# Optimization experiments

Hardware: AMD Instinct MI355X
Metric: run time of the kernel (lower is better)

The kernel has to match this reference:

```python
import jax, jax.numpy as jnp
import numpy as np

D_MODEL = 768
N_HEADS = 8
D_K = D_MODEL // N_HEADS
D_FF = 2048
EPS = 1e-5


def _layer_norm(x, gamma, beta):
    mu = jnp.mean(x, axis=-1, keepdims=True)
    var = jnp.mean(jnp.square(x - mu), axis=-1, keepdims=True)
    return (x - mu) * jax.lax.rsqrt(var + EPS) * gamma + beta


def setup_inputs() -> dict:
    key = jax.random.key(0)
    ks = jax.random.split(key, 16)
    s = 1.0 / np.sqrt(D_MODEL)
    sf = 1.0 / np.sqrt(D_FF)
    inp = {
        "x": jax.random.normal(ks[0], (4, 2048, D_MODEL), jnp.float32),
        "Wq": jax.random.uniform(ks[1], (D_MODEL, D_MODEL), jnp.float32, -s, s),
        "bq": jnp.zeros((D_MODEL,), jnp.float32),
        "Wk": jax.random.uniform(ks[2], (D_MODEL, D_MODEL), jnp.float32, -s, s),
        "bk": jnp.zeros((D_MODEL,), jnp.float32),
        "Wv": jax.random.uniform(ks[3], (D_MODEL, D_MODEL), jnp.float32, -s, s),
        "bv": jnp.zeros((D_MODEL,), jnp.float32),
        "Wo": jax.random.uniform(ks[4], (D_MODEL, D_MODEL), jnp.float32, -s, s),
        "bo": jnp.zeros((D_MODEL,), jnp.float32),
        "g1": jnp.ones((D_MODEL,), jnp.float32),
        "be1": jnp.zeros((D_MODEL,), jnp.float32),
        "W1": jax.random.uniform(ks[5], (D_MODEL, D_FF), jnp.float32, -s, s),
        "b1": jnp.zeros((D_FF,), jnp.float32),
        "W2": jax.random.uniform(ks[6], (D_FF, D_MODEL), jnp.float32, -sf, sf),
        "b2": jnp.zeros((D_MODEL,), jnp.float32),
        "g2": jnp.ones((D_MODEL,), jnp.float32),
        "be2": jnp.zeros((D_MODEL,), jnp.float32),
    }
    return inp


def reference(x, Wq, bq, Wk, bk, Wv, bv, Wo, bo, g1, be1, W1, b1, W2, b2, g2, be2):
    B, S, D = x.shape
    residual = x
    # projections, split into heads: [B, H, S, d_k]
    def proj(W, b):
        return (x @ W + b).reshape(B, S, N_HEADS, D_K).transpose(0, 2, 1, 3)
    Q, K, V = proj(Wq, bq), proj(Wk, bk), proj(Wv, bv)
    # explicit (non-fused) attention, as in the original
    scores = jnp.einsum('bhqd,bhkd->bhqk', Q, K) / np.sqrt(D_K)  # [B,H,S,S]
    attn = jax.nn.softmax(scores, axis=-1)
    out = jnp.einsum('bhqk,bhkd->bhqd', attn, V)
    out = out.transpose(0, 2, 1, 3).reshape(B, S, D)
    out = out @ Wo + bo
    x1 = _layer_norm(residual + out, g1, be1)
    ff = jax.nn.relu(x1 @ W1 + b1) @ W2 + b2
    return _layer_norm(x1 + ff, g2, be2)
```

## Files before the change

kernel.cpp:

```cpp
#include <hip/hip_runtime.h>
#include <cstdint>
#include <cstddef>

typedef unsigned short u16;
typedef __bf16 bf16x8 __attribute__((ext_vector_type(8)));
typedef float f32x4 __attribute__((ext_vector_type(4)));

#define BATCH 4
#define SEQ   2048
#define DM    768
#define NH    8
#define DK    96
#define DFF   2048
#define MTOK  8192
#define QKVN  2304
#define LOG2E 1.44269504088896340736f

__device__ __forceinline__ u16 f2bf(float f) {
  union { float f; uint32_t u; } v; v.f = f;
  return (u16)((v.u + 0x7fffu + ((v.u >> 16) & 1u)) >> 16);
}
__device__ __forceinline__ float bf2f(u16 b) {
  union { uint32_t u; float f; } v; v.u = (uint32_t)b << 16;
  return v.f;
}
__device__ __forceinline__ bf16x8 ld8(const u16* p) { return *(const bf16x8*)p; }
__device__ __forceinline__ void async16(const u16* g, u16* l) {
  __builtin_amdgcn_global_load_lds((const __attribute__((address_space(1))) void*)g,
                                   (__attribute__((address_space(3))) void*)l, 16, 0, 0);
}

__global__ __launch_bounds__(256)
void prep(const float* __restrict__ x, u16* __restrict__ xb,
          const float* __restrict__ bq, const float* __restrict__ bk,
          const float* __restrict__ bv, float* __restrict__ bqkv,
          const float* __restrict__ Wq, const float* __restrict__ Wk,
          const float* __restrict__ Wv, const float* __restrict__ Wo,
          const float* __restrict__ W1, const float* __restrict__ W2,
          u16* __restrict__ WT, u16* __restrict__ WoT,
          u16* __restrict__ W1T, u16* __restrict__ W2T) {
  __shared__ float t[32][33];
  const int tid = threadIdx.x;
  int bid = blockIdx.x;

  if (bid < 6144) {
    size_t i = (size_t)bid * 1024 + tid * 4;
    float4 f = *(const float4*)(x + i);
    uint2 o;
    o.x = (unsigned)f2bf(f.x) | ((unsigned)f2bf(f.y) << 16);
    o.y = (unsigned)f2bf(f.z) | ((unsigned)f2bf(f.w) << 16);
    *(uint2*)(xb + i) = o;
    return;
  }
  if (bid < 6153) {
    int i = (bid - 6144) * 256 + tid;
    float v = (i < 768) ? bq[i] : (i < 1536) ? bk[i - 768] : bv[i - 1536];
    bqkv[i] = v;
    return;
  }
  bid -= 6153;
  const float* in; u16* out; int C, R, bx, by;
  if (bid < 576)       { in = Wq; out = WT;                 C = 768;  R = 768;  bx = bid % 24;          by = bid / 24; }
  else if (bid < 1152) { in = Wk; out = WT + 768 * 768;     C = 768;  R = 768;  bx = (bid - 576) % 24;  by = (bid - 576) / 24; }
  else if (bid < 1728) { in = Wv; out = WT + 2 * 768 * 768; C = 768;  R = 768;  bx = (bid - 1152) % 24; by = (bid - 1152) / 24; }
  else if (bid < 2304) { in = Wo; out = WoT;                C = 768;  R = 768;  bx = (bid - 1728) % 24; by = (bid - 1728) / 24; }
  else if (bid < 3840) { in = W1; out = W1T;                C = 2048; R = 768;  bx = (bid - 2304) % 64; by = (bid - 2304) / 64; }
  else                 { in = W2; out = W2T;                C = 768;  R = 2048; bx = (bid - 3840) % 24; by = (bid - 3840) / 24; }
  const int r0 = by * 32, c0 = bx * 32;
  const int tx = tid & 31, ty = tid >> 5;
#pragma unroll
  for (int i = 0; i < 4; i++)
    t[ty + i * 8][tx] = in[(size_t)(r0 + ty + i * 8) * C + c0 + tx];
  __syncthreads();
#pragma unroll
  for (int i = 0; i < 4; i++)
    out[(size_t)(c0 + ty + i * 8) * R + r0 + tx] = f2bf(t[tx][ty + i * 8]);
}

__global__ void transpose_v(const u16* __restrict__ v, u16* __restrict__ vt) {
  __shared__ u16 t[32][33];
  int bh = blockIdx.z, b = bh >> 3, h = bh & 7;
  int s0 = blockIdx.x * 32, d0 = blockIdx.y * 32;
  int tx = threadIdx.x, ty = threadIdx.y;
#pragma unroll
  for (int i = 0; i < 4; i++)
    t[ty + i * 8][tx] = v[(size_t)(b * SEQ + s0 + ty + i * 8) * QKVN + h * DK + d0 + tx];
  __syncthreads();
#pragma unroll
  for (int i = 0; i < 4; i++)
    vt[(size_t)(bh * DK + d0 + ty + i * 8) * SEQ + s0 + tx] = t[tx][ty + i * 8];
}

template <int RESID, int RELU, int OUTBF>
__global__ __launch_bounds__(256, 4)
void gemm_bt(const u16* __restrict__ A, const u16* __restrict__ BT,
             const float* __restrict__ bias, const float* __restrict__ resid,
             float* __restrict__ Cf, u16* __restrict__ Cb, int N, int K) {
  __shared__ __align__(16) u16 lA[128 * 64];
  __shared__ __align__(16) u16 lB[128 * 64];
  const int tid = threadIdx.x;
  const int wave = tid >> 6, lane = tid & 63;
  const int quad = lane >> 4, l16 = lane & 15;
  const int wm = wave >> 1, wn = wave & 1;
  const int tm = blockIdx.y * 128, tn = blockIdx.x * 128;

  f32x4 acc[4][4] = {};

  for (int k0 = 0; k0 < K; k0 += 64) {
    __syncthreads();
#pragma unroll
    for (int i = 0; i < 4; i++) {
      int cbase = (wave * 4 + i) * 64;
      int c = cbase + lane;
      int row = c >> 3;
      int scc = (c & 7) ^ (row & 7);
      async16(A + (size_t)(tm + row) * K + k0 + scc * 8, &lA[cbase * 8]);
      async16(BT + (size_t)(tn + row) * K + k0 + scc * 8, &lB[cbase * 8]);
    }
    __syncthreads();
#pragma unroll
    for (int ks = 0; ks < 2; ks++) {
      bf16x8 af[4], bfr[4];
#pragma unroll
      for (int i = 0; i < 4; i++) {
        int ra = wm * 64 + i * 16 + l16;
        af[i] = ld8(&lA[ra * 64 + (((ks * 4 + quad) ^ (ra & 7)) << 3)]);
        int rb = wn * 64 + i * 16 + l16;
        bfr[i] = ld8(&lB[rb * 64 + (((ks * 4 + quad) ^ (rb & 7)) << 3)]);
      }
#pragma unroll
      for (int i = 0; i < 4; i++)
#pragma unroll
        for (int j = 0; j < 4; j++)
          acc[i][j] = __builtin_amdgcn_mfma_f32_16x16x32_bf16(af[i], bfr[j], acc[i][j], 0, 0, 0);
    }
  }

#pragma unroll
  for (int i = 0; i < 4; i++) {
    const int row0 = tm + wm * 64 + i * 16 + quad * 4;
#pragma unroll
    for (int j = 0; j < 4; j++) {
      const int col = tn + wn * 64 + j * 16 + l16;
      const float bv = bias[col];
#pragma unroll
      for (int r = 0; r < 4; r++) {
        float v = acc[i][j][r] + bv;
        if (RESID) v += resid[(size_t)(row0 + r) * N + col];
        if (RELU) v = fmaxf(v, 0.f);
        if (OUTBF) Cb[(size_t)(row0 + r) * N + col] = f2bf(v);
        else       Cf[(size_t)(row0 + r) * N + col] = v;
      }
    }
  }
}

template <int RESID, int RELU, int OUTBF, int RESBF>
__global__ __launch_bounds__(256, 4)
void gemm_bt64(const u16* __restrict__ A, const u16* __restrict__ BT,
               const float* __restrict__ bias, const float* __restrict__ residf,
               const u16* __restrict__ residb,
               float* __restrict__ Cf, u16* __restrict__ Cb, int N, int K) {
  __shared__ __align__(16) u16 lA[128 * 64];
  __shared__ __align__(16) u16 lB[64 * 64];
  const int tid = threadIdx.x;
  const int wave = tid >> 6, lane = tid & 63;
  const int quad = lane >> 4, l16 = lane & 15;
  const int wm = wave >> 1, wn = wave & 1;
  const int tm = blockIdx.y * 128, tn = blockIdx.x * 64;

  f32x4 acc[4][2] = {};

  for (int k0 = 0; k0 < K; k0 += 64) {
    __syncthreads();
#pragma unroll
    for (int i = 0; i < 4; i++) {
      int cbase = (wave * 4 + i) * 64;
      int c = cbase + lane;
      int row = c >> 3;
      int scc = (c & 7) ^ (row & 7);
      async16(A + (size_t)(tm + row) * K + k0 + scc * 8, &lA[cbase * 8]);
    }
#pragma unroll
    for (int i = 0; i < 2; i++) {
      int cbase = (wave * 2 + i) * 64;
      int c = cbase + lane;
      int row = c >> 3;
      int scc = (c & 7) ^ (row & 7);
      async16(BT + (size_t)(tn + row) * K + k0 + scc * 8, &lB[cbase * 8]);
    }
    __syncthreads();
#pragma unroll
    for (int ks = 0; ks < 2; ks++) {
      bf16x8 af[4], bfr[2];
#pragma unroll
      for (int i = 0; i < 4; i++) {
        int ra = wm * 64 + i * 16 + l16;
        af[i] = ld8(&lA[ra * 64 + (((ks * 4 + quad) ^ (ra & 7)) << 3)]);
      }
#pragma unroll
      for (int j = 0; j < 2; j++) {
        int rb = wn * 32 + j * 16 + l16;
        bfr[j] = ld8(&lB[rb * 64 + (((ks * 4 + quad) ^ (rb & 7)) << 3)]);
      }
#pragma unroll
      for (int i = 0; i < 4; i++)
#pragma unroll
        for (int j = 0; j < 2; j++)
          acc[i][j] = __builtin_amdgcn_mfma_f32_16x16x32_bf16(af[i], bfr[j], acc[i][j], 0, 0, 0);
    }
  }

#pragma unroll
  for (int i = 0; i < 4; i++) {
    const int row0 = tm + wm * 64 + i * 16 + quad * 4;
#pragma unroll
    for (int j = 0; j < 2; j++) {
      const int col = tn + wn * 32 + j * 16 + l16;
      const float bv = bias[col];
#pragma unroll
      for (int r = 0; r < 4; r++) {
        float v = acc[i][j][r] + bv;
        if (RESID) {
          if (RESBF) v += bf2f(residb[(size_t)(row0 + r) * N + col]);
          else       v += residf[(size_t)(row0 + r) * N + col];
        }
        if (RELU) v = fmaxf(v, 0.f);
        if (OUTBF) Cb[(size_t)(row0 + r) * N + col] = f2bf(v);
        else       Cf[(size_t)(row0 + r) * N + col] = v;
      }
    }
  }
}

#define LKW 128
#define LVW 64
#define LPP 44
__global__ __launch_bounds__(256)
void flash_attn(const u16* __restrict__ qkv, const u16* __restrict__ Vt,
                u16* __restrict__ Ob) {
  __shared__ __align__(16) u16 lK[2][64 * LKW];
  __shared__ __align__(16) u16 lV[2][96 * LVW];
  __shared__ __align__(16) u16 lP[4][32 * LPP];
  const int tid = threadIdx.x, wave = tid >> 6, lane = tid & 63;
  const int quad = lane >> 4, l16 = lane & 15;
  const int lin = blockIdx.x;
  const int bh = (lin & 7) * 4 + ((lin >> 3) & 3);
  const int qb = lin >> 5;
  const int b = bh >> 3, h = bh & 7;
  const int q0 = qb * 128 + wave * 32;
  const u16* Qp = qkv;
  const u16* KpB = qkv + 768 + (size_t)b * SEQ * QKVN + h * DK;
  const u16* VtB = Vt + (size_t)bh * DK * SEQ;
  const float cs = 0.10206207262f * LOG2E;
  const float Ms = 16.0f * cs;

  bf16x8 qf[2][3];
#pragma unroll
  for (int mi = 0; mi < 2; mi++)
#pragma unroll
    for (int ks = 0; ks < 3; ks++)
      qf[mi][ks] = ld8(Qp + (size_t)(b * SEQ + q0 + mi * 16 + l16) * QKVN +
                       h * DK + ks * 32 + quad * 8);

  union { u16 u[8]; bf16x8 v; } onesu;
#pragma unroll
  for (int i = 0; i < 8; i++) onesu.u[i] = 0x3F80;
  const bf16x8 onef = onesu.v;

  f32x4 of[2][6] = {};
  f32x4 l_acc[2] = {};
  u16* pw = lP[wave];

  auto stage = [&](int kt, int buf) {
#pragma unroll
    for (int i = 0; i < 4; i++) {
      int s = i * 256 + tid;
      int row = s >> 4;
      int c = (s & 15) ^ (row & 7);
      if (c > 11) c = 11;
      async16(KpB + (size_t)(kt + row) * QKVN + c * 8,
              &lK[buf][(i * 256 + wave * 64) * 8]);
    }
#pragma unroll
    for (int i = 0; i < 3; i++) {
      int s = i * 256 + tid;
      int row = s >> 3;
      int c = (s & 7) ^ (row & 7);
      async16(VtB + (size_t)row * SEQ + kt + c * 8,
              &lV[buf][(i * 256 + wave * 64) * 8]);
    }
  };

  stage(0, 0);
  int cur = 0;

  for (int kt = 0; kt < SEQ; kt += 64) {
    __syncthreads();
    if (kt + 64 < SEQ) stage(kt + 64, cur ^ 1);

    f32x4 sc[2][4] = {};
#pragma unroll
    for (int ks = 0; ks < 3; ks++) {
      bf16x8 kb[4];
#pragma unroll
      for (int ni = 0; ni < 4; ni++)
        kb[ni] = ld8(&lK[cur][(ni * 16 + l16) * LKW +
                             (((ks * 4 + quad) ^ (l16 & 7)) << 3)]);
#pragma unroll
      for (int mi = 0; mi < 2; mi++)
#pragma unroll
        for (int ni = 0; ni < 4; ni++)
          sc[mi][ni] = __builtin_amdgcn_mfma_f32_16x16x32_bf16(qf[mi][ks], kb[ni], sc[mi][ni], 0, 0, 0);
    }

#pragma unroll
    for (int mi = 0; mi < 2; mi++)
#pragma unroll
      for (int ni = 0; ni < 4; ni++)
#pragma unroll
        for (int r = 0; r < 4; r++) {
          float p = __builtin_amdgcn_exp2f(sc[mi][ni][r] * cs - Ms);
          union { float f; uint32_t u; } pu; pu.f = p;
          pw[(mi * 16 + quad * 4 + r) * LPP + ni * 16 + l16] =
              (u16)((pu.u + 0x8000u) >> 16);
        }

#pragma unroll
    for (int ks = 0; ks < 2; ks++) {
      bf16x8 pa[2];
#pragma unroll
      for (int mi = 0; mi < 2; mi++) {
        pa[mi] = ld8(&pw[(mi * 16 + l16) * LPP + ks * 32 + quad * 8]);
        l_acc[mi] = __builtin_amdgcn_mfma_f32_16x16x32_bf16(pa[mi], onef, l_acc[mi], 0, 0, 0);
      }
#pragma unroll
      for (int j = 0; j < 6; j++) {
        bf16x8 vb = ld8(&lV[cur][(j * 16 + l16) * LVW +
                                 (((ks * 4 + quad) ^ (l16 & 7)) << 3)]);
#pragma unroll
        for (int mi = 0; mi < 2; mi++)
          of[mi][j] = __builtin_amdgcn_mfma_f32_16x16x32_bf16(pa[mi], vb, of[mi][j], 0, 0, 0);
      }
    }
    cur ^= 1;
  }

#pragma unroll
  for (int mi = 0; mi < 2; mi++)
#pragma unroll
    for (int r = 0; r < 4; r++) {
      float inv = 1.f / l_acc[mi][r];
      int qrow = q0 + mi * 16 + quad * 4 + r;
#pragma unroll
      for (int j = 0; j < 6; j++)
        Ob[(size_t)(b * SEQ + qrow) * DM + h * DK + j * 16 + l16] = f2bf(of[mi][j][r] * inv);
    }
}

__global__ __launch_bounds__(256)
void ln_kernel(const float* __restrict__ y, const float* __restrict__ g,
               const float* __restrict__ be, float* __restrict__ outf,
               u16* __restrict__ outb) {
  int row = blockIdx.x, t = threadIdx.x;
  const float* yr = y + (size_t)row * DM;
  float v[3], s = 0.f, s2 = 0.f;
#pragma unroll
  for (int i = 0; i < 3; i++) {
    v[i] = yr[t + i * 256];
    s += v[i];
    s2 += v[i] * v[i];
  }
#pragma unroll
  for (int m = 1; m < 64; m <<= 1) {
    s += __shfl_xor(s, m);
    s2 += __shfl_xor(s2, m);
  }
  __shared__ float red[2][4];
  int w = t >> 6;
  if ((t & 63) == 0) { red[0][w] = s; red[1][w] = s2; }
  __syncthreads();
  s = red[0][0] + red[0][1] + red[0][2] + red[0][3];
  s2 = red[1][0] + red[1][1] + red[1][2] + red[1][3];
  float mu = s * (1.f / DM);
  float var = s2 * (1.f / DM) - mu * mu;
  float rs = rsqrtf(var + 1e-5f);
#pragma unroll
  for (int i = 0; i < 3; i++) {
    int e = t + i * 256;
    float o = (v[i] - mu) * rs * g[e] + be[e];
    if (outf) outf[(size_t)row * DM + e] = o;
    if (outb) outb[(size_t)row * DM + e] = f2bf(o);
  }
}

#define SZ_BF 12582912ull
#define SZ_F  25165824ull
#define O_XB   0ull
#define O_WT   (O_XB + SZ_BF)
#define O_WOT  (O_WT + 3538944ull)
#define O_W1T  (O_WOT + 1179648ull)
#define O_W2T  (O_W1T + 3145728ull)
#define O_QKV  (O_W2T + 3145728ull)
#define O_VT   (O_QKV + 37748736ull)
#define O_Y    (O_VT + SZ_BF)
#define O_X1F  (O_Y + SZ_F)
#define O_BIAS (O_X1F + SZ_F)

extern "C" void kernel_launch(void* const* d_in, const int* in_sizes, int n_in,
                              void* d_out, int out_size, void* d_ws, size_t ws_size,
                              hipStream_t stream) {
  const float* x   = (const float*)d_in[0];
  const float* Wq  = (const float*)d_in[1];
  const float* bq  = (const float*)d_in[2];
  const float* Wk  = (const float*)d_in[3];
  const float* bk  = (const float*)d_in[4];
  const float* Wv  = (const float*)d_in[5];
  const float* bv  = (const float*)d_in[6];
  const float* Wo  = (const float*)d_in[7];
  const float* bo  = (const float*)d_in[8];
  const float* g1  = (const float*)d_in[9];
  const float* be1 = (const float*)d_in[10];
  const float* W1  = (const float*)d_in[11];
  const float* b1  = (const float*)d_in[12];
  const float* W2  = (const float*)d_in[13];
  const float* b2  = (const float*)d_in[14];
  const float* g2  = (const float*)d_in[15];
  const float* be2 = (const float*)d_in[16];
  float* out = (float*)d_out;
  char* ws = (char*)d_ws;

  u16* xb    = (u16*)(ws + O_XB);
  u16* WT    = (u16*)(ws + O_WT);
  u16* WoT   = (u16*)(ws + O_WOT);
  u16* W1T   = (u16*)(ws + O_W1T);
  u16* W2T   = (u16*)(ws + O_W2T);
  u16* qkv   = (u16*)(ws + O_QKV);
  u16* vt    = (u16*)(ws + O_VT);
  float* y   = (float*)(ws + O_Y);
  float* bqkv = (float*)(ws + O_BIAS);
  u16* ao   = xb;
  u16* x1b  = qkv;
  u16* hbuf = qkv + (size_t)MTOK * DM;

  prep<<<11529, 256, 0, stream>>>(x, xb, bq, bk, bv, bqkv,
                                  Wq, Wk, Wv, Wo, W1, W2,
                                  WT, WoT, W1T, W2T);

  gemm_bt<0, 0, 1><<<dim3(18, 64), 256, 0, stream>>>(xb, WT, bqkv, nullptr, nullptr, qkv, QKVN, DM);
  transpose_v<<<dim3(64, 3, 32), dim3(32, 8), 0, stream>>>(qkv + 1536, vt);
  flash_attn<<<512, 256, 0, stream>>>(qkv, vt, ao);
  gemm_bt64<1, 0, 0, 0><<<dim3(12, 64), 256, 0, stream>>>(ao, WoT, bo, x, nullptr, y, nullptr, DM, DM);
  ln_kernel<<<8192, 256, 0, stream>>>(y, g1, be1, nullptr, x1b);
  gemm_bt<0, 1, 1><<<dim3(16, 64), 256, 0, stream>>>(x1b, W1T, b1, nullptr, nullptr, hbuf, DFF, DM);
  gemm_bt64<1, 0, 0, 1><<<dim3(12, 64), 256, 0, stream>>>(hbuf, W2T, b2, nullptr, x1b, y, nullptr, DM, DFF);
  ln_kernel<<<8192, 256, 0, stream>>>(y, g2, be2, out, nullptr);
}
```

Baseline: 379.4 us.

## Split attention over key halves with 8-wave blocks and a combine kernel

```diff
diff --git a/kernel.cpp b/kernel.cpp
--- a/kernel.cpp
+++ b/kernel.cpp
@@ -236,19 +236,21 @@
 #define LKW 128
 #define LVW 64
 #define LPP 44
-__global__ __launch_bounds__(256)
+__global__ __launch_bounds__(512, 4)
 void flash_attn(const u16* __restrict__ qkv, const u16* __restrict__ Vt,
-                u16* __restrict__ Ob) {
+                float* __restrict__ Opart, float* __restrict__ Lpart) {
   __shared__ __align__(16) u16 lK[2][64 * LKW];
   __shared__ __align__(16) u16 lV[2][96 * LVW];
-  __shared__ __align__(16) u16 lP[4][32 * LPP];
+  __shared__ __align__(16) u16 lP[8][32 * LPP];
   const int tid = threadIdx.x, wave = tid >> 6, lane = tid & 63;
   const int quad = lane >> 4, l16 = lane & 15;
   const int lin = blockIdx.x;
   const int bh = (lin & 7) * 4 + ((lin >> 3) & 3);
-  const int qb = lin >> 5;
+  const int qb = (lin >> 5) & 7;
+  const int kh = lin >> 8;
   const int b = bh >> 3, h = bh & 7;
-  const int q0 = qb * 128 + wave * 32;
+  const int q0 = qb * 256 + wave * 32;
+  const int k_lo = kh * 1024;
   const u16* Qp = qkv;
   const u16* KpB = qkv + 768 + (size_t)b * SEQ * QKVN + h * DK;
   const u16* VtB = Vt + (size_t)bh * DK * SEQ;
@@ -274,30 +276,36 @@
 
   auto stage = [&](int kt, int buf) {
 #pragma unroll
-    for (int i = 0; i < 4; i++) {
-      int s = i * 256 + tid;
+    for (int i = 0; i < 2; i++) {
+      int s = i * 512 + tid;
       int row = s >> 4;
       int c = (s & 15) ^ (row & 7);
       if (c > 11) c = 11;
       async16(KpB + (size_t)(kt + row) * QKVN + c * 8,
-              &lK[buf][(i * 256 + wave * 64) * 8]);
-    }
-#pragma unroll
-    for (int i = 0; i < 3; i++) {
-      int s = i * 256 + tid;
+              &lK[buf][(i * 512 + wave * 64) * 8]);
+    }
+    {
+      int s = tid;
       int row = s >> 3;
       int c = (s & 7) ^ (row & 7);
       async16(VtB + (size_t)row * SEQ + kt + c * 8,
-              &lV[buf][(i * 256 + wave * 64) * 8]);
+              &lV[buf][(wave * 64) * 8]);
+    }
+    if (wave < 4) {
+      int s = 512 + tid;
+      int row = s >> 3;
+      int c = (s & 7) ^ (row & 7);
+      async16(VtB + (size_t)row * SEQ + kt + c * 8,
+              &lV[buf][(512 + wave * 64) * 8]);
     }
   };
 
-  stage(0, 0);
+  stage(k_lo, 0);
   int cur = 0;
 
-  for (int kt = 0; kt < SEQ; kt += 64) {
+  for (int kt = k_lo; kt < k_lo + 1024; kt += 64) {
     __syncthreads();
-    if (kt + 64 < SEQ) stage(kt + 64, cur ^ 1);
+    if (kt + 64 < k_lo + 1024) stage(kt + 64, cur ^ 1);
 
     f32x4 sc[2][4] = {};
 #pragma unroll
@@ -307,11 +315,13 @@
       for (int ni = 0; ni < 4; ni++)
         kb[ni] = ld8(&lK[cur][(ni * 16 + l16) * LKW +
                              (((ks * 4 + quad) ^ (l16 & 7)) << 3)]);
+      __builtin_amdgcn_s_setprio(1);
 #pragma unroll
       for (int mi = 0; mi < 2; mi++)
 #pragma unroll
         for (int ni = 0; ni < 4; ni++)
           sc[mi][ni] = __builtin_amdgcn_mfma_f32_16x16x32_bf16(qf[mi][ks], kb[ni], sc[mi][ni], 0, 0, 0);
+      __builtin_amdgcn_s_setprio(0);
     }
 
 #pragma unroll
@@ -334,6 +344,7 @@
         pa[mi] = ld8(&pw[(mi * 16 + l16) * LPP + ks * 32 + quad * 8]);
         l_acc[mi] = __builtin_amdgcn_mfma_f32_16x16x32_bf16(pa[mi], onef, l_acc[mi], 0, 0, 0);
       }
+      __builtin_amdgcn_s_setprio(1);
 #pragma unroll
       for (int j = 0; j < 6; j++) {
         bf16x8 vb = ld8(&lV[cur][(j * 16 + l16) * LVW +
@@ -342,6 +353,7 @@
         for (int mi = 0; mi < 2; mi++)
           of[mi][j] = __builtin_amdgcn_mfma_f32_16x16x32_bf16(pa[mi], vb, of[mi][j], 0, 0, 0);
       }
+      __builtin_amdgcn_s_setprio(0);
     }
     cur ^= 1;
   }
@@ -350,12 +362,33 @@
   for (int mi = 0; mi < 2; mi++)
 #pragma unroll
     for (int r = 0; r < 4; r++) {
-      float inv = 1.f / l_acc[mi][r];
       int qrow = q0 + mi * 16 + quad * 4 + r;
+      size_t base = ((size_t)(kh * 32 + bh) * SEQ + qrow) * DK;
 #pragma unroll
       for (int j = 0; j < 6; j++)
-        Ob[(size_t)(b * SEQ + qrow) * DM + h * DK + j * 16 + l16] = f2bf(of[mi][j][r] * inv);
-    }
+        Opart[base + j * 16 + l16] = of[mi][j][r];
+      if (l16 == 0)
+        Lpart[(size_t)(kh * 32 + bh) * SEQ + qrow] = l_acc[mi][r];
+    }
+}
+
+__global__ __launch_bounds__(256)
+void attn_combine(const float* __restrict__ Op, const float* __restrict__ Lp,
+                  u16* __restrict__ Ob) {
+  const int bh = blockIdx.y, b = bh >> 3, h = bh & 7;
+  const int flat = blockIdx.x * 256 + threadIdx.x;
+  const int q = flat / 24, dq = (flat % 24) * 4;
+  const size_t i0 = ((size_t)bh * SEQ + q) * DK + dq;
+  const size_t i1 = ((size_t)(32 + bh) * SEQ + q) * DK + dq;
+  float4 o0 = *(const float4*)(Op + i0);
+  float4 o1 = *(const float4*)(Op + i1);
+  float inv = 1.f / (Lp[(size_t)bh * SEQ + q] + Lp[(size_t)(32 + bh) * SEQ + q]);
+  uint2 o;
+  o.x = (unsigned)f2bf((o0.x + o1.x) * inv) |
+        ((unsigned)f2bf((o0.y + o1.y) * inv) << 16);
+  o.y = (unsigned)f2bf((o0.z + o1.z) * inv) |
+        ((unsigned)f2bf((o0.w + o1.w) * inv) << 16);
+  *(uint2*)(Ob + (size_t)(b * SEQ + q) * DM + h * DK + dq) = o;
 }
 
 __global__ __launch_bounds__(256)
@@ -442,6 +475,8 @@
   u16* ao   = xb;
   u16* x1b  = qkv;
   u16* hbuf = qkv + (size_t)MTOK * DM;
+  float* opart = (float*)(ws + O_Y);
+  float* lpart = (float*)(ws + O_WT);
 
   prep<<<11529, 256, 0, stream>>>(x, xb, bq, bk, bv, bqkv,
                                   Wq, Wk, Wv, Wo, W1, W2,
@@ -449,7 +484,8 @@
 
   gemm_bt<0, 0, 1><<<dim3(18, 64), 256, 0, stream>>>(xb, WT, bqkv, nullptr, nullptr, qkv, QKVN, DM);
   transpose_v<<<dim3(64, 3, 32), dim3(32, 8), 0, stream>>>(qkv + 1536, vt);
-  flash_attn<<<512, 256, 0, stream>>>(qkv, vt, ao);
+  flash_attn<<<512, 512, 0, stream>>>(qkv, vt, opart, lpart);
+  attn_combine<<<dim3(192, 32), 256, 0, stream>>>(opart, lpart, ao);
   gemm_bt64<1, 0, 0, 0><<<dim3(12, 64), 256, 0, stream>>>(ao, WoT, bo, x, nullptr, y, nullptr, DM, DM);
   ln_kernel<<<8192, 256, 0, stream>>>(y, g1, be1, nullptr, x1b);
   gemm_bt<0, 1, 1><<<dim3(16, 64), 256, 0, stream>>>(x1b, W1T, b1, nullptr, nullptr, hbuf, DFF, DM);
```

Result: slower. 412.6 us (+8.8%).

## Split flash attention across 8 waves of 16 query rows with MFMA priority

Applied to the files above, without the earlier changes.

```diff
diff --git a/kernel.cpp b/kernel.cpp
--- a/kernel.cpp
+++ b/kernel.cpp
@@ -236,59 +236,63 @@
 #define LKW 128
 #define LVW 64
 #define LPP 44
-__global__ __launch_bounds__(256)
+__global__ __launch_bounds__(512, 4)
 void flash_attn(const u16* __restrict__ qkv, const u16* __restrict__ Vt,
                 u16* __restrict__ Ob) {
   __shared__ __align__(16) u16 lK[2][64 * LKW];
   __shared__ __align__(16) u16 lV[2][96 * LVW];
-  __shared__ __align__(16) u16 lP[4][32 * LPP];
+  __shared__ __align__(16) u16 lP[8][16 * LPP];
   const int tid = threadIdx.x, wave = tid >> 6, lane = tid & 63;
   const int quad = lane >> 4, l16 = lane & 15;
   const int lin = blockIdx.x;
   const int bh = (lin & 7) * 4 + ((lin >> 3) & 3);
   const int qb = lin >> 5;
   const int b = bh >> 3, h = bh & 7;
-  const int q0 = qb * 128 + wave * 32;
+  const int q0 = qb * 128 + wave * 16;
   const u16* Qp = qkv;
   const u16* KpB = qkv + 768 + (size_t)b * SEQ * QKVN + h * DK;
   const u16* VtB = Vt + (size_t)bh * DK * SEQ;
   const float cs = 0.10206207262f * LOG2E;
   const float Ms = 16.0f * cs;
 
-  bf16x8 qf[2][3];
-#pragma unroll
-  for (int mi = 0; mi < 2; mi++)
-#pragma unroll
-    for (int ks = 0; ks < 3; ks++)
-      qf[mi][ks] = ld8(Qp + (size_t)(b * SEQ + q0 + mi * 16 + l16) * QKVN +
-                       h * DK + ks * 32 + quad * 8);
+  bf16x8 qf[3];
+#pragma unroll
+  for (int ks = 0; ks < 3; ks++)
+    qf[ks] = ld8(Qp + (size_t)(b * SEQ + q0 + l16) * QKVN +
+                 h * DK + ks * 32 + quad * 8);
 
   union { u16 u[8]; bf16x8 v; } onesu;
 #pragma unroll
   for (int i = 0; i < 8; i++) onesu.u[i] = 0x3F80;
   const bf16x8 onef = onesu.v;
 
-  f32x4 of[2][6] = {};
-  f32x4 l_acc[2] = {};
+  f32x4 of[6] = {};
+  f32x4 l_acc = {};
   u16* pw = lP[wave];
 
   auto stage = [&](int kt, int buf) {
 #pragma unroll
-    for (int i = 0; i < 4; i++) {
-      int s = i * 256 + tid;
+    for (int i = 0; i < 2; i++) {
+      int s = i * 512 + tid;
       int row = s >> 4;
       int c = (s & 15) ^ (row & 7);
       if (c > 11) c = 11;
       async16(KpB + (size_t)(kt + row) * QKVN + c * 8,
-              &lK[buf][(i * 256 + wave * 64) * 8]);
-    }
-#pragma unroll
-    for (int i = 0; i < 3; i++) {
-      int s = i * 256 + tid;
+              &lK[buf][(i * 512 + wave * 64) * 8]);
+    }
+    {
+      int s = tid;
       int row = s >> 3;
       int c = (s & 7) ^ (row & 7);
       async16(VtB + (size_t)row * SEQ + kt + c * 8,
-              &lV[buf][(i * 256 + wave * 64) * 8]);
+              &lV[buf][(wave * 64) * 8]);
+    }
+    if (wave < 4) {
+      int s = 512 + tid;
+      int row = s >> 3;
+      int c = (s & 7) ^ (row & 7);
+      async16(VtB + (size_t)row * SEQ + kt + c * 8,
+              &lV[buf][(512 + wave * 64) * 8]);
     }
   };
 
@@ -299,7 +303,7 @@
     __syncthreads();
     if (kt + 64 < SEQ) stage(kt + 64, cur ^ 1);
 
-    f32x4 sc[2][4] = {};
+    f32x4 sc[4] = {};
 #pragma unroll
     for (int ks = 0; ks < 3; ks++) {
       bf16x8 kb[4];
@@ -307,55 +311,47 @@
       for (int ni = 0; ni < 4; ni++)
         kb[ni] = ld8(&lK[cur][(ni * 16 + l16) * LKW +
                              (((ks * 4 + quad) ^ (l16 & 7)) << 3)]);
-#pragma unroll
-      for (int mi = 0; mi < 2; mi++)
-#pragma unroll
-        for (int ni = 0; ni < 4; ni++)
-          sc[mi][ni] = __builtin_amdgcn_mfma_f32_16x16x32_bf16(qf[mi][ks], kb[ni], sc[mi][ni], 0, 0, 0);
-    }
-
-#pragma unroll
-    for (int mi = 0; mi < 2; mi++)
+      __builtin_amdgcn_s_setprio(1);
 #pragma unroll
       for (int ni = 0; ni < 4; ni++)
-#pragma unroll
-        for (int r = 0; r < 4; r++) {
-          float p = __builtin_amdgcn_exp2f(sc[mi][ni][r] * cs - Ms);
-          union { float f; uint32_t u; } pu; pu.f = p;
-          pw[(mi * 16 + quad * 4 + r) * LPP + ni * 16 + l16] =
-              (u16)((pu.u + 0x8000u) >> 16);
-        }
+        sc[ni] = __builtin_amdgcn_mfma_f32_16x16x32_bf16(qf[ks], kb[ni], sc[ni], 0, 0, 0);
+      __builtin_amdgcn_s_setprio(0);
+    }
+
+#pragma unroll
+    for (int ni = 0; ni < 4; ni++)
+#pragma unroll
+      for (int r = 0; r < 4; r++) {
+        float p = __builtin_amdgcn_exp2f(sc[ni][r] * cs - Ms);
+        union { float f; uint32_t u; } pu; pu.f = p;
+        pw[(quad * 4 + r) * LPP + ni * 16 + l16] =
+            (u16)((pu.u + 0x8000u) >> 16);
+      }
 
 #pragma unroll
     for (int ks = 0; ks < 2; ks++) {
-      bf16x8 pa[2];
-#pragma unroll
-      for (int mi = 0; mi < 2; mi++) {
-        pa[mi] = ld8(&pw[(mi * 16 + l16) * LPP + ks * 32 + quad * 8]);
-        l_acc[mi] = __builtin_amdgcn_mfma_f32_16x16x32_bf16(pa[mi], onef, l_acc[mi], 0, 0, 0);
-      }
+      bf16x8 pa = ld8(&pw[l16 * LPP + ks * 32 + quad * 8]);
+      l_acc = __builtin_amdgcn_mfma_f32_16x16x32_bf16(pa, onef, l_acc, 0, 0, 0);
+      __builtin_amdgcn_s_setprio(1);
 #pragma unroll
       for (int j = 0; j < 6; j++) {
         bf16x8 vb = ld8(&lV[cur][(j * 16 + l16) * LVW +
                                  (((ks * 4 + quad) ^ (l16 & 7)) << 3)]);
-#pragma unroll
-        for (int mi = 0; mi < 2; mi++)
-          of[mi][j] = __builtin_amdgcn_mfma_f32_16x16x32_bf16(pa[mi], vb, of[mi][j], 0, 0, 0);
-      }
+        of[j] = __builtin_amdgcn_mfma_f32_16x16x32_bf16(pa, vb, of[j], 0, 0, 0);
+      }
+      __builtin_amdgcn_s_setprio(0);
     }
     cur ^= 1;
   }
 
 #pragma unroll
-  for (int mi = 0; mi < 2; mi++)
-#pragma unroll
-    for (int r = 0; r < 4; r++) {
-      float inv = 1.f / l_acc[mi][r];
-      int qrow = q0 + mi * 16 + quad * 4 + r;
-#pragma unroll
-      for (int j = 0; j < 6; j++)
-        Ob[(size_t)(b * SEQ + qrow) * DM + h * DK + j * 16 + l16] = f2bf(of[mi][j][r] * inv);
-    }
+  for (int r = 0; r < 4; r++) {
+    float inv = 1.f / l_acc[r];
+    int qrow = q0 + quad * 4 + r;
+#pragma unroll
+    for (int j = 0; j < 6; j++)
+      Ob[(size_t)(b * SEQ + qrow) * DM + h * DK + j * 16 + l16] = f2bf(of[j][r] * inv);
+  }
 }
 
 __global__ __launch_bounds__(256)
@@ -449,7 +445,7 @@
 
   gemm_bt<0, 0, 1><<<dim3(18, 64), 256, 0, stream>>>(xb, WT, bqkv, nullptr, nullptr, qkv, QKVN, DM);
   transpose_v<<<dim3(64, 3, 32), dim3(32, 8), 0, stream>>>(qkv + 1536, vt);
-  flash_attn<<<512, 256, 0, stream>>>(qkv, vt, ao);
+  flash_attn<<<512, 512, 0, stream>>>(qkv, vt, ao);
   gemm_bt64<1, 0, 0, 0><<<dim3(12, 64), 256, 0, stream>>>(ao, WoT, bo, x, nullptr, y, nullptr, DM, DM);
   ln_kernel<<<8192, 256, 0, stream>>>(y, g1, be1, nullptr, x1b);
   gemm_bt<0, 1, 1><<<dim3(16, 64), 256, 0, stream>>>(x1b, W1T, b1, nullptr, nullptr, hbuf, DFF, DM);
```

Result: no change. 384.7 us (+1.4%).

## Rewrite flash attention with transposed 32x32 MFMA and register-resident P

Applied to the files above, without the earlier changes.

```diff
diff --git a/kernel.cpp b/kernel.cpp
--- a/kernel.cpp
+++ b/kernel.cpp
@@ -5,6 +5,7 @@
 typedef unsigned short u16;
 typedef __bf16 bf16x8 __attribute__((ext_vector_type(8)));
 typedef float f32x4 __attribute__((ext_vector_type(4)));
+typedef float f32x16 __attribute__((ext_vector_type(16)));
 
 #define BATCH 4
 #define SEQ   2048
@@ -235,15 +236,28 @@
 
 #define LKW 128
 #define LVW 64
-#define LPP 44
+
+#define PACK_SLICE(SC, B, DST)                                                   \
+  {                                                                              \
+    uint32_t u0, u1, u2, u3;                                                     \
+    asm("v_cvt_pk_bf16_f32 %0, %1, %2" : "=v"(u0) : "v"(SC[B+0]), "v"(SC[B+1])); \
+    asm("v_cvt_pk_bf16_f32 %0, %1, %2" : "=v"(u1) : "v"(SC[B+2]), "v"(SC[B+3])); \
+    asm("v_cvt_pk_bf16_f32 %0, %1, %2" : "=v"(u2) : "v"(SC[B+4]), "v"(SC[B+5])); \
+    asm("v_cvt_pk_bf16_f32 %0, %1, %2" : "=v"(u3) : "v"(SC[B+6]), "v"(SC[B+7])); \
+    asm("v_permlane32_swap_b32 %0, %1" : "+v"(u2), "+v"(u0));                    \
+    asm("v_permlane32_swap_b32 %0, %1" : "+v"(u3), "+v"(u1));                    \
+    union { uint32_t w[4]; bf16x8 v; } pu_;                                      \
+    pu_.w[0] = u0; pu_.w[1] = u1; pu_.w[2] = u2; pu_.w[3] = u3;                  \
+    DST = pu_.v;                                                                 \
+  }
+
 __global__ __launch_bounds__(256)
 void flash_attn(const u16* __restrict__ qkv, const u16* __restrict__ Vt,
                 u16* __restrict__ Ob) {
   __shared__ __align__(16) u16 lK[2][64 * LKW];
   __shared__ __align__(16) u16 lV[2][96 * LVW];
-  __shared__ __align__(16) u16 lP[4][32 * LPP];
   const int tid = threadIdx.x, wave = tid >> 6, lane = tid & 63;
-  const int quad = lane >> 4, l16 = lane & 15;
+  const int l32 = lane & 31, half = lane >> 5, l7 = lane & 7;
   const int lin = blockIdx.x;
   const int bh = (lin & 7) * 4 + ((lin >> 3) & 3);
   const int qb = lin >> 5;
@@ -255,22 +269,13 @@
   const float cs = 0.10206207262f * LOG2E;
   const float Ms = 16.0f * cs;
 
-  bf16x8 qf[2][3];
-#pragma unroll
-  for (int mi = 0; mi < 2; mi++)
-#pragma unroll
-    for (int ks = 0; ks < 3; ks++)
-      qf[mi][ks] = ld8(Qp + (size_t)(b * SEQ + q0 + mi * 16 + l16) * QKVN +
-                       h * DK + ks * 32 + quad * 8);
-
-  union { u16 u[8]; bf16x8 v; } onesu;
-#pragma unroll
-  for (int i = 0; i < 8; i++) onesu.u[i] = 0x3F80;
-  const bf16x8 onef = onesu.v;
-
-  f32x4 of[2][6] = {};
-  f32x4 l_acc[2] = {};
-  u16* pw = lP[wave];
+  bf16x8 qf[6];
+#pragma unroll
+  for (int d = 0; d < 6; d++)
+    qf[d] = ld8(Qp + (size_t)(b * SEQ + q0 + l32) * QKVN + h * DK + d * 16 + half * 8);
+
+  f32x16 of[3] = {};
+  float l_lane = 0.f;
 
   auto stage = [&](int kt, int buf) {
 #pragma unroll
@@ -299,62 +304,57 @@
     __syncthreads();
     if (kt + 64 < SEQ) stage(kt + 64, cur ^ 1);
 
-    f32x4 sc[2][4] = {};
-#pragma unroll
-    for (int ks = 0; ks < 3; ks++) {
-      bf16x8 kb[4];
-#pragma unroll
-      for (int ni = 0; ni < 4; ni++)
-        kb[ni] = ld8(&lK[cur][(ni * 16 + l16) * LKW +
-                             (((ks * 4 + quad) ^ (l16 & 7)) << 3)]);
-#pragma unroll
-      for (int mi = 0; mi < 2; mi++)
-#pragma unroll
-        for (int ni = 0; ni < 4; ni++)
-          sc[mi][ni] = __builtin_amdgcn_mfma_f32_16x16x32_bf16(qf[mi][ks], kb[ni], sc[mi][ni], 0, 0, 0);
-    }
-
-#pragma unroll
-    for (int mi = 0; mi < 2; mi++)
-#pragma unroll
-      for (int ni = 0; ni < 4; ni++)
-#pragma unroll
-        for (int r = 0; r < 4; r++) {
-          float p = __builtin_amdgcn_exp2f(sc[mi][ni][r] * cs - Ms);
-          union { float f; uint32_t u; } pu; pu.f = p;
-          pw[(mi * 16 + quad * 4 + r) * LPP + ni * 16 + l16] =
-              (u16)((pu.u + 0x8000u) >> 16);
-        }
-
-#pragma unroll
-    for (int ks = 0; ks < 2; ks++) {
-      bf16x8 pa[2];
-#pragma unroll
-      for (int mi = 0; mi < 2; mi++) {
-        pa[mi] = ld8(&pw[(mi * 16 + l16) * LPP + ks * 32 + quad * 8]);
-        l_acc[mi] = __builtin_amdgcn_mfma_f32_16x16x32_bf16(pa[mi], onef, l_acc[mi], 0, 0, 0);
-      }
-#pragma unroll
-      for (int j = 0; j < 6; j++) {
-        bf16x8 vb = ld8(&lV[cur][(j * 16 + l16) * LVW +
-                                 (((ks * 4 + quad) ^ (l16 & 7)) << 3)]);
-#pragma unroll
-        for (int mi = 0; mi < 2; mi++)
-          of[mi][j] = __builtin_amdgcn_mfma_f32_16x16x32_bf16(pa[mi], vb, of[mi][j], 0, 0, 0);
-      }
-    }
+    f32x16 sc0 = {}, sc1 = {};
+    __builtin_amdgcn_s_setprio(1);
+#pragma unroll
+    for (int d = 0; d < 6; d++) {
+      const int sl = ((d * 2 + half) ^ l7) << 3;
+      bf16x8 k0 = ld8(&lK[cur][l32 * LKW + sl]);
+      bf16x8 k1 = ld8(&lK[cur][(32 + l32) * LKW + sl]);
+      sc0 = __builtin_amdgcn_mfma_f32_32x32x16_bf16(k0, qf[d], sc0, 0, 0, 0);
+      sc1 = __builtin_amdgcn_mfma_f32_32x32x16_bf16(k1, qf[d], sc1, 0, 0, 0);
+    }
+    __builtin_amdgcn_s_setprio(0);
+
+#pragma unroll
+    for (int r = 0; r < 16; r++) {
+      float p0 = __builtin_amdgcn_exp2f(sc0[r] * cs - Ms);
+      float p1 = __builtin_amdgcn_exp2f(sc1[r] * cs - Ms);
+      l_lane += p0 + p1;
+      sc0[r] = p0;
+      sc1[r] = p1;
+    }
+
+    bf16x8 pa[4];
+    PACK_SLICE(sc0, 0, pa[0])
+    PACK_SLICE(sc0, 8, pa[1])
+    PACK_SLICE(sc1, 0, pa[2])
+    PACK_SLICE(sc1, 8, pa[3])
+
+    __builtin_amdgcn_s_setprio(1);
+#pragma unroll
+    for (int ks = 0; ks < 4; ks++) {
+      const int sl = ((ks * 2 + half) ^ l7) << 3;
+#pragma unroll
+      for (int db = 0; db < 3; db++) {
+        bf16x8 va = ld8(&lV[cur][(db * 32 + l32) * LVW + sl]);
+        of[db] = __builtin_amdgcn_mfma_f32_32x32x16_bf16(va, pa[ks], of[db], 0, 0, 0);
+      }
+    }
+    __builtin_amdgcn_s_setprio(0);
     cur ^= 1;
   }
 
-#pragma unroll
-  for (int mi = 0; mi < 2; mi++)
-#pragma unroll
-    for (int r = 0; r < 4; r++) {
-      float inv = 1.f / l_acc[mi][r];
-      int qrow = q0 + mi * 16 + quad * 4 + r;
-#pragma unroll
-      for (int j = 0; j < 6; j++)
-        Ob[(size_t)(b * SEQ + qrow) * DM + h * DK + j * 16 + l16] = f2bf(of[mi][j][r] * inv);
+  float lt = l_lane + __shfl_xor(l_lane, 32);
+  float inv = 1.f / lt;
+  const int q = q0 + l32;
+  u16* Orow = Ob + (size_t)(b * SEQ + q) * DM + h * DK;
+#pragma unroll
+  for (int db = 0; db < 3; db++)
+#pragma unroll
+    for (int r = 0; r < 16; r++) {
+      int dk = db * 32 + (r & 3) + 8 * (r >> 2) + 4 * half;
+      Orow[dk] = f2bf(of[db][r] * inv);
     }
 }
 
```

New measurement: 345.3 us. -9.0%, faster.
